# Kernel tuning notes

Hardware: AMD Instinct MI355X
Metric: run time of the kernel (lower is better)

## Reference

```python
import jax, jax.numpy as jnp
import numpy as np

B, T, IN, OUT, R = 4096, 8, 1024, 1024, 32

def setup_inputs() -> dict:
    key = jax.random.key(0)
    k1, k2, k3, k4 = jax.random.split(key, 4)
    return {
        "x": jax.random.normal(k1, (B, T, IN), dtype=jnp.float32),
        "first_shared_core": jax.random.normal(k2, (T, R), dtype=jnp.float32) * 0.1,
        "middle_shared_core": jax.random.normal(k3, (R, IN, R), dtype=jnp.float32) * 0.1,
        "task_core": jax.random.normal(k4, (R, OUT), dtype=jnp.float32) * 0.1,
    }

def reference(x, first_shared_core, middle_shared_core, task_core):
    # contract TT cores -> per-task weight [T, IN, OUT]
    w = jnp.einsum('tj,jik->tik', first_shared_core, middle_shared_core)
    w = jnp.einsum('tik,ko->tio', w, task_core)
    # per-task batched matmul: [B,T,IN] x [T,IN,OUT] -> [B,T,OUT]
    return jnp.einsum('bti,tio->bto', x, w)
```

## Files before the change

### kernel.cpp

```cpp
#include <hip/hip_runtime.h>
#include <hip/hip_bf16.h>
#include <stdint.h>

#define B_DIM 4096
#define T_DIM 8
#define IN_DIM 1024
#define OUT_DIM 1024
#define R_DIM 32

#define BM 128
#define BN 128
#define BK 64
#define NKT (IN_DIM / BK)

typedef __bf16 bf16x8 __attribute__((ext_vector_type(8)));
typedef float  f32x4  __attribute__((ext_vector_type(4)));


__device__ __forceinline__ uint32_t pack2_bf16(float a, float b) {
  uint32_t ua = __float_as_uint(a), ub = __float_as_uint(b);
  ua = (ua + 0x7FFFu + ((ua >> 16) & 1u)) >> 16;
  ub = (ub + 0x7FFFu + ((ub >> 16) & 1u)) & 0xFFFF0000u;
  return ua | ub;
}

__device__ __forceinline__ void gload_lds16(const void* g, void* l) {
  __builtin_amdgcn_global_load_lds(
      (const __attribute__((address_space(1))) void*)(uintptr_t)g,
      (__attribute__((address_space(3))) void*)(uint32_t)(uintptr_t)l,
      16, 0, 0);
}

__global__ void tt_stage1(const float* __restrict__ first,
                          const float* __restrict__ middle,
                          float* __restrict__ a1) {
  int idx = blockIdx.x * 256 + threadIdx.x;
  int t  = idx >> 15;
  int ik = idx & 32767;
  float acc = 0.f;
#pragma unroll
  for (int j = 0; j < R_DIM; ++j)
    acc = fmaf(first[t * R_DIM + j], middle[j * (IN_DIM * R_DIM) + ik], acc);
  a1[idx] = acc;
}

__global__ __launch_bounds__(256) void tt_stage2(const float* __restrict__ a1,
                                                 const float* __restrict__ task,
                                                 __hip_bfloat16* __restrict__ wT) {
  int bid = blockIdx.x;
  int t  = bid >> 8;
  int ob = (bid >> 4) & 15;
  int ib = bid & 15;
  __shared__ float A1s[64][33];
  __shared__ float Ts[32][64];
  int tid = threadIdx.x;
#pragma unroll
  for (int r = 0; r < 8; ++r) {
    int idx2 = tid + 256 * r;
    int il = idx2 >> 5, k = idx2 & 31;
    A1s[il][k] = a1[t * (IN_DIM * R_DIM) + (ib * 64 + il) * R_DIM + k];
  }
#pragma unroll
  for (int r = 0; r < 8; ++r) {
    int idx2 = tid + 256 * r;
    int k = idx2 >> 6, ol = idx2 & 63;
    Ts[k][ol] = task[k * OUT_DIM + ob * 64 + ol];
  }
  __syncthreads();
  int il = tid & 63;
  int og = tid >> 6;
  float acc[16];
#pragma unroll
  for (int r = 0; r < 16; ++r) acc[r] = 0.f;
#pragma unroll
  for (int k = 0; k < 32; ++k) {
    float a = A1s[il][k];
#pragma unroll
    for (int r = 0; r < 16; ++r)
      acc[r] = fmaf(a, Ts[k][og * 16 + r], acc[r]);
  }
#pragma unroll
  for (int r = 0; r < 16; ++r) {
    size_t o = (size_t)ob * 64 + og * 16 + r;
    wT[((size_t)t * OUT_DIM + o) * IN_DIM + ib * 64 + il] = __float2bfloat16(acc[r]);
  }
}

__global__ __launch_bounds__(256, 3) void tt_gemm(const float* __restrict__ X,
                                                  const uint16_t* __restrict__ WT,
                                                  float* __restrict__ O) {
  extern __shared__ uint8_t sm[];

  const int cpx = (T_DIM * (B_DIM / BM) * (OUT_DIM / BN)) >> 3;
  int bid = blockIdx.x;
  int l  = (bid & 7) * cpx + (bid >> 3);
  int t  = l >> 8;
  int mt = (l >> 3) & 31;
  int nt = l & 7;

  const int tid  = threadIdx.x;
  const int lane = tid & 63;
  const int wave = tid >> 6;
  const int wr = wave >> 1, wc = wave & 1;

  const int a_row  = tid >> 4;
  const int a_col4 = tid & 15;
  const float* xbase =
      X + ((size_t)(mt * BM) * T_DIM + t) * IN_DIM + a_col4 * 4;

  const int b_rowin = lane >> 3;
  const int b_c     = lane & 7;
  const int b_gcol  = (b_c * 16) ^ (b_rowin << 4);
  const uint16_t* wtile = WT + ((size_t)(t * OUT_DIM + nt * BN)) * IN_DIM;

  const int r0a  = wr * 64 + (lane & 15);
  const int r0b  = wc * 64 + (lane & 15);
  const int kswz = (lane & 7) << 4;
  const int kg   = lane >> 4;

  f32x4 acc[4][4] = {};
  float4 areg[8];

#pragma unroll
  for (int r = 0; r < 8; ++r)
    areg[r] = *(const float4*)(xbase + (size_t)(a_row + 16 * r) * (T_DIM * IN_DIM));

  for (int kt = 0; kt < NKT; ++kt) {
#pragma unroll
    for (int r = 0; r < 8; ++r) {
      int row = a_row + 16 * r;
      uint2 v;
      v.x = pack2_bf16(areg[r].x, areg[r].y);
      v.y = pack2_bf16(areg[r].z, areg[r].w);
      *(uint2*)(sm + row * 128 + ((a_col4 * 8) ^ ((row & 7) << 4))) = v;
    }
    {
      const uint16_t* wk = wtile + (size_t)kt * BK;
#pragma unroll
      for (int q = 0; q < 4; ++q) {
        int row = (wave * 4 + q) * 8 + b_rowin;
        gload_lds16((const uint8_t*)(wk + (size_t)row * IN_DIM) + b_gcol,
                    sm + 16384 + (wave * 4 + q) * 1024);
      }
    }
    __syncthreads();

    if (kt + 1 < NKT) {
      const float* xk = xbase + (size_t)(kt + 1) * BK;
#pragma unroll
      for (int r = 0; r < 8; ++r)
        areg[r] = *(const float4*)(xk + (size_t)(a_row + 16 * r) * (T_DIM * IN_DIM));
    }

    const uint8_t* ab = sm;
    const uint8_t* bb = sm + 16384;
#pragma unroll
    for (int ks = 0; ks < 2; ++ks) {
      const int kbyte = (ks * 64 + kg * 16) ^ kswz;
      bf16x8 af[4], bfr[4];
#pragma unroll
      for (int m = 0; m < 4; ++m)
        af[m] = *(const bf16x8*)(ab + (r0a + m * 16) * 128 + kbyte);
#pragma unroll
      for (int n = 0; n < 4; ++n)
        bfr[n] = *(const bf16x8*)(bb + (r0b + n * 16) * 128 + kbyte);
#pragma unroll
      for (int m = 0; m < 4; ++m)
#pragma unroll
        for (int n = 0; n < 4; ++n)
          acc[m][n] = __builtin_amdgcn_mfma_f32_16x16x32_bf16(af[m], bfr[n],
                                                              acc[m][n], 0, 0, 0);
    }
    __syncthreads();
  }

  const size_t obase =
      (size_t)(mt * BM) * (T_DIM * OUT_DIM) + (size_t)t * OUT_DIM + nt * BN;
  const int crow0 = wr * 64 + (lane >> 4) * 4;
  const int ccol  = wc * 64 + (lane & 15);
#pragma unroll
  for (int m = 0; m < 4; ++m) {
#pragma unroll
    for (int j = 0; j < 4; ++j) {
      size_t rowoff = obase + (size_t)(crow0 + m * 16 + j) * (T_DIM * OUT_DIM) + ccol;
#pragma unroll
      for (int n = 0; n < 4; ++n)
        O[rowoff + n * 16] = acc[m][n][j];
    }
  }
}

extern "C" void kernel_launch(void* const* d_in, const int* in_sizes, int n_in,
                              void* d_out, int out_size, void* d_ws, size_t ws_size,
                              hipStream_t stream) {
  const float* x      = (const float*)d_in[0];
  const float* first  = (const float*)d_in[1];
  const float* middle = (const float*)d_in[2];
  const float* task   = (const float*)d_in[3];
  float* out = (float*)d_out;

  float* a1 = (float*)d_ws;
  __hip_bfloat16* wT = (__hip_bfloat16*)((uint8_t*)d_ws + (1u << 20));

  tt_stage1<<<(T_DIM * IN_DIM * R_DIM) / 256, 256, 0, stream>>>(first, middle, a1);
  tt_stage2<<<T_DIM * 16 * 16, 256, 0, stream>>>(a1, task, wT);
  tt_gemm<<<T_DIM * (B_DIM / BM) * (OUT_DIM / BN), 256, 32768, stream>>>(
      x, (const uint16_t*)wT, out);
}
```

Baseline: 144.2 us.

## Stream fp32 X tiles directly to LDS and convert to bf16 at fragment load

The A operand (fp32 activations) is no longer loaded into registers, converted and written to LDS. It is now copied straight into a swizzled fp32 LDS tile with global_load_lds, and truncated to bf16 via byte-permute when each MFMA fragment is read. This removes the register staging and the round-to-nearest conversion from the load path. In exchange it doubles LDS use for A (48KB total), which may cut occupancy below the 3 blocks requested. It also drops the register prefetch of the next tile, and truncation replaces rounding, which slightly changes numerics.

```diff
diff --git a/kernel.cpp b/kernel.cpp
--- a/kernel.cpp
+++ b/kernel.cpp
@@ -16,13 +16,6 @@
 typedef __bf16 bf16x8 __attribute__((ext_vector_type(8)));
 typedef float  f32x4  __attribute__((ext_vector_type(4)));
 
-
-__device__ __forceinline__ uint32_t pack2_bf16(float a, float b) {
-  uint32_t ua = __float_as_uint(a), ub = __float_as_uint(b);
-  ua = (ua + 0x7FFFu + ((ua >> 16) & 1u)) >> 16;
-  ub = (ub + 0x7FFFu + ((ub >> 16) & 1u)) & 0xFFFF0000u;
-  return ua | ub;
-}
 
 __device__ __forceinline__ void gload_lds16(const void* g, void* l) {
   __builtin_amdgcn_global_load_lds(
@@ -103,67 +96,64 @@
   const int wave = tid >> 6;
   const int wr = wave >> 1, wc = wave & 1;
 
-  const int a_row  = tid >> 4;
-  const int a_col4 = tid & 15;
-  const float* xbase =
-      X + ((size_t)(mt * BM) * T_DIM + t) * IN_DIM + a_col4 * 4;
+  const int a_lrow   = lane >> 4;
+  const int a_lchunk = lane & 15;
+  const int srcf0 = (a_lchunk ^ a_lrow) * 4;
+  const int srcf1 = (a_lchunk ^ (4 + a_lrow)) * 4;
+  const float* xrow =
+      X + (size_t)(mt * BM + wave * 32 + a_lrow) * (T_DIM * IN_DIM) + t * IN_DIM;
 
   const int b_rowin = lane >> 3;
-  const int b_c     = lane & 7;
-  const int b_gcol  = (b_c * 16) ^ (b_rowin << 4);
+  const int b_gcol  = ((lane & 7) * 16) ^ (b_rowin << 4);
   const uint16_t* wtile = WT + ((size_t)(t * OUT_DIM + nt * BN)) * IN_DIM;
 
-  const int r0a  = wr * 64 + (lane & 15);
-  const int r0b  = wc * 64 + (lane & 15);
-  const int kswz = (lane & 7) << 4;
-  const int kg   = lane >> 4;
+  const int r0a = wr * 64 + (lane & 15);
+  const int r0b = wc * 64 + (lane & 15);
+  const int sA  = lane & 7;
+  const int kg  = lane >> 4;
+  const int kswzB = (lane & 7) << 4;
 
   f32x4 acc[4][4] = {};
-  float4 areg[8];
-
-#pragma unroll
-  for (int r = 0; r < 8; ++r)
-    areg[r] = *(const float4*)(xbase + (size_t)(a_row + 16 * r) * (T_DIM * IN_DIM));
 
   for (int kt = 0; kt < NKT; ++kt) {
+    const float* xk = xrow + kt * BK;
 #pragma unroll
-    for (int r = 0; r < 8; ++r) {
-      int row = a_row + 16 * r;
-      uint2 v;
-      v.x = pack2_bf16(areg[r].x, areg[r].y);
-      v.y = pack2_bf16(areg[r].z, areg[r].w);
-      *(uint2*)(sm + row * 128 + ((a_col4 * 8) ^ ((row & 7) << 4))) = v;
+    for (int qq = 0; qq < 8; ++qq) {
+      gload_lds16(xk + (size_t)qq * 4 * (T_DIM * IN_DIM) + ((qq & 1) ? srcf1 : srcf0),
+                  sm + (wave * 8 + qq) * 1024);
     }
-    {
-      const uint16_t* wk = wtile + (size_t)kt * BK;
+    const uint16_t* wk = wtile + (size_t)kt * BK;
 #pragma unroll
-      for (int q = 0; q < 4; ++q) {
-        int row = (wave * 4 + q) * 8 + b_rowin;
-        gload_lds16((const uint8_t*)(wk + (size_t)row * IN_DIM) + b_gcol,
-                    sm + 16384 + (wave * 4 + q) * 1024);
-      }
+    for (int q = 0; q < 4; ++q) {
+      int row = (wave * 4 + q) * 8 + b_rowin;
+      gload_lds16((const uint8_t*)(wk + (size_t)row * IN_DIM) + b_gcol,
+                  sm + 32768 + (wave * 4 + q) * 1024);
     }
     __syncthreads();
 
-    if (kt + 1 < NKT) {
-      const float* xk = xbase + (size_t)(kt + 1) * BK;
-#pragma unroll
-      for (int r = 0; r < 8; ++r)
-        areg[r] = *(const float4*)(xk + (size_t)(a_row + 16 * r) * (T_DIM * IN_DIM));
-    }
-
     const uint8_t* ab = sm;
-    const uint8_t* bb = sm + 16384;
+    const uint8_t* bb = sm + 32768;
 #pragma unroll
     for (int ks = 0; ks < 2; ++ks) {
-      const int kbyte = (ks * 64 + kg * 16) ^ kswz;
       bf16x8 af[4], bfr[4];
 #pragma unroll
-      for (int m = 0; m < 4; ++m)
-        af[m] = *(const bf16x8*)(ab + (r0a + m * 16) * 128 + kbyte);
+      for (int m = 0; m < 4; ++m) {
+        const int row = r0a + m * 16;
+        const int c0  = ks * 8 + kg * 2;
+        f32x4 lo = *(const f32x4*)(ab + row * 256 + (((c0    ) ^ sA) << 4));
+        f32x4 hi = *(const f32x4*)(ab + row * 256 + (((c0 + 1) ^ sA) << 4));
+        union { uint32_t u[4]; bf16x8 v; } cv;
+        cv.u[0] = __builtin_amdgcn_perm(__float_as_uint(lo.y), __float_as_uint(lo.x), 0x07060302u);
+        cv.u[1] = __builtin_amdgcn_perm(__float_as_uint(lo.w), __float_as_uint(lo.z), 0x07060302u);
+        cv.u[2] = __builtin_amdgcn_perm(__float_as_uint(hi.y), __float_as_uint(hi.x), 0x07060302u);
+        cv.u[3] = __builtin_amdgcn_perm(__float_as_uint(hi.w), __float_as_uint(hi.z), 0x07060302u);
+        af[m] = cv.v;
+      }
 #pragma unroll
-      for (int n = 0; n < 4; ++n)
+      for (int n = 0; n < 4; ++n) {
+        const int kbyte = (ks * 64 + kg * 16) ^ kswzB;
         bfr[n] = *(const bf16x8*)(bb + (r0b + n * 16) * 128 + kbyte);
+      }
 #pragma unroll
       for (int m = 0; m < 4; ++m)
 #pragma unroll
@@ -204,6 +194,6 @@
 
   tt_stage1<<<(T_DIM * IN_DIM * R_DIM) / 256, 256, 0, stream>>>(first, middle, a1);
   tt_stage2<<<T_DIM * 16 * 16, 256, 0, stream>>>(a1, task, wT);
-  tt_gemm<<<T_DIM * (B_DIM / BM) * (OUT_DIM / BN), 256, 32768, stream>>>(
+  tt_gemm<<<T_DIM * (B_DIM / BM) * (OUT_DIM / BN), 256, 49152, stream>>>(
       x, (const uint16_t*)wT, out);
 }
```

Result: faster. 139.5 us (-3.3%).

## Pre-convert X to bf16 and use 256x256 double-buffered 8-wave GEMM pipeline

Applied to the files above, without the earlier changes.

Adds a separate kernel that converts X to bf16 in a transposed [T,B,IN] layout, so the GEMM can load both operands straight into LDS with global_load_lds. The GEMM moves to 256x256 tiles with 8 waves and double-buffered 128KB LDS. Each k-step is split into four quadrant phases that interleave async loads for the next tile with MFMA bursts, using explicit vmcnt waits, barriers and setprio. The aim is to hide global-load latency and raise operand reuse per tile. In exchange it adds a full extra read and write pass over X and far fewer, larger workgroups (512 blocks).

```diff
diff --git a/kernel.cpp b/kernel.cpp
--- a/kernel.cpp
+++ b/kernel.cpp
@@ -8,13 +8,17 @@
 #define OUT_DIM 1024
 #define R_DIM 32
 
-#define BM 128
-#define BN 128
+#define BM 256
+#define BN 256
 #define BK 64
 #define NKT (IN_DIM / BK)
 
 typedef __bf16 bf16x8 __attribute__((ext_vector_type(8)));
 typedef float  f32x4  __attribute__((ext_vector_type(4)));
+
+#define VMCNT(n) asm volatile("s_waitcnt vmcnt(" #n ")" ::: "memory")
+#define CFENCE() asm volatile("" ::: "memory")
+#define BARRIER() do { CFENCE(); __builtin_amdgcn_s_barrier(); CFENCE(); } while (0)
 
 
 __device__ __forceinline__ uint32_t pack2_bf16(float a, float b) {
@@ -29,6 +33,43 @@
       (const __attribute__((address_space(1))) void*)(uintptr_t)g,
       (__attribute__((address_space(3))) void*)(uint32_t)(uintptr_t)l,
       16, 0, 0);
+}
+
+__device__ __forceinline__ void stage_half(const uint16_t* gtile, int ktn,
+                                           int half, uint8_t* ldsop,
+                                           int wave, int lane) {
+#pragma unroll
+  for (int j = 0; j < 2; ++j) {
+    int s = j * 64 + wave * 8 + (lane >> 3);
+    int c = lane & 7;
+    int row = (s >> 4) * 32 + half * 16 + (s & 15);
+    gload_lds16((const uint8_t*)(gtile + (size_t)row * IN_DIM + ktn * BK) +
+                    ((c ^ (s & 7)) << 4),
+                ldsop + half * 16384 + j * 8192 + wave * 1024);
+  }
+}
+
+__device__ __forceinline__ bf16x8 lds_frag(const uint8_t* op, int grp ,
+                                           int par , int ks,
+                                           int l15, int kg, int l7) {
+  return *(const bf16x8*)(op + par * 16384 + (grp >> 1) * 2048 + l15 * 128 +
+                          ((((ks << 2) + kg) ^ l7) << 4));
+}
+
+__global__ __launch_bounds__(256) void x_cvt(const float* __restrict__ x,
+                                             uint16_t* __restrict__ xb) {
+  int u = blockIdx.x * 256 + threadIdx.x;
+  int i0 = (u & 127) << 3;
+  int bt = u >> 7;
+  int t = bt & 7, b = bt >> 3;
+  const float4* src = (const float4*)(x + (size_t)bt * IN_DIM + i0);
+  float4 v0 = src[0], v1 = src[1];
+  uint4 o;
+  o.x = pack2_bf16(v0.x, v0.y);
+  o.y = pack2_bf16(v0.z, v0.w);
+  o.z = pack2_bf16(v1.x, v1.y);
+  o.w = pack2_bf16(v1.z, v1.w);
+  *(uint4*)(xb + ((size_t)t * B_DIM + b) * IN_DIM + i0) = o;
 }
 
 __global__ void tt_stage1(const float* __restrict__ first,
@@ -86,103 +127,132 @@
   }
 }
 
-__global__ __launch_bounds__(256, 3) void tt_gemm(const float* __restrict__ X,
+__global__ __launch_bounds__(512, 2) void tt_gemm(const uint16_t* __restrict__ XB,
                                                   const uint16_t* __restrict__ WT,
                                                   float* __restrict__ O) {
   extern __shared__ uint8_t sm[];
-
-  const int cpx = (T_DIM * (B_DIM / BM) * (OUT_DIM / BN)) >> 3;
   int bid = blockIdx.x;
-  int l  = (bid & 7) * cpx + (bid >> 3);
-  int t  = l >> 8;
-  int mt = (l >> 3) & 31;
-  int nt = l & 7;
+  const int t  = bid & 7;
+  const int l  = bid >> 3;
+  const int mt = l >> 2;
+  const int nt = l & 3;
 
   const int tid  = threadIdx.x;
   const int lane = tid & 63;
   const int wave = tid >> 6;
-  const int wr = wave >> 1, wc = wave & 1;
-
-  const int a_row  = tid >> 4;
-  const int a_col4 = tid & 15;
-  const float* xbase =
-      X + ((size_t)(mt * BM) * T_DIM + t) * IN_DIM + a_col4 * 4;
-
-  const int b_rowin = lane >> 3;
-  const int b_c     = lane & 7;
-  const int b_gcol  = (b_c * 16) ^ (b_rowin << 4);
-  const uint16_t* wtile = WT + ((size_t)(t * OUT_DIM + nt * BN)) * IN_DIM;
-
-  const int r0a  = wr * 64 + (lane & 15);
-  const int r0b  = wc * 64 + (lane & 15);
-  const int kswz = (lane & 7) << 4;
-  const int kg   = lane >> 4;
-
-  f32x4 acc[4][4] = {};
-  float4 areg[8];
-
-#pragma unroll
-  for (int r = 0; r < 8; ++r)
-    areg[r] = *(const float4*)(xbase + (size_t)(a_row + 16 * r) * (T_DIM * IN_DIM));
-
+  const int wr = wave >> 2, wc = wave & 3;
+  const int wr8 = wr * 8, wc4 = wc * 4;
+  const int l15 = lane & 15, l7 = lane & 7, kg = lane >> 4;
+
+  const uint16_t* gA = XB + ((size_t)t * B_DIM + mt * BM) * IN_DIM;
+  const uint16_t* gB = WT + ((size_t)t * OUT_DIM + nt * BN) * IN_DIM;
+
+  f32x4 acc[8][4] = {};
+  bf16x8 afr[4][2], bfr0[2][2], bfr1[2][2];
+
+  stage_half(gA, 0, 0, sm, wave, lane);
+  stage_half(gB, 0, 0, sm + 32768, wave, lane);
+  stage_half(gA, 0, 1, sm, wave, lane);
+  stage_half(gB, 0, 1, sm + 32768, wave, lane);
+  VMCNT(0);
+  BARRIER();
+
+#pragma unroll 2
   for (int kt = 0; kt < NKT; ++kt) {
-#pragma unroll
-    for (int r = 0; r < 8; ++r) {
-      int row = a_row + 16 * r;
-      uint2 v;
-      v.x = pack2_bf16(areg[r].x, areg[r].y);
-      v.y = pack2_bf16(areg[r].z, areg[r].w);
-      *(uint2*)(sm + row * 128 + ((a_col4 * 8) ^ ((row & 7) << 4))) = v;
-    }
-    {
-      const uint16_t* wk = wtile + (size_t)kt * BK;
-#pragma unroll
-      for (int q = 0; q < 4; ++q) {
-        int row = (wave * 4 + q) * 8 + b_rowin;
-        gload_lds16((const uint8_t*)(wk + (size_t)row * IN_DIM) + b_gcol,
-                    sm + 16384 + (wave * 4 + q) * 1024);
-      }
-    }
-    __syncthreads();
-
-    if (kt + 1 < NKT) {
-      const float* xk = xbase + (size_t)(kt + 1) * BK;
-#pragma unroll
-      for (int r = 0; r < 8; ++r)
-        areg[r] = *(const float4*)(xk + (size_t)(a_row + 16 * r) * (T_DIM * IN_DIM));
-    }
-
-    const uint8_t* ab = sm;
-    const uint8_t* bb = sm + 16384;
-#pragma unroll
-    for (int ks = 0; ks < 2; ++ks) {
-      const int kbyte = (ks * 64 + kg * 16) ^ kswz;
-      bf16x8 af[4], bfr[4];
-#pragma unroll
-      for (int m = 0; m < 4; ++m)
-        af[m] = *(const bf16x8*)(ab + (r0a + m * 16) * 128 + kbyte);
-#pragma unroll
-      for (int n = 0; n < 4; ++n)
-        bfr[n] = *(const bf16x8*)(bb + (r0b + n * 16) * 128 + kbyte);
-#pragma unroll
-      for (int m = 0; m < 4; ++m)
-#pragma unroll
-        for (int n = 0; n < 4; ++n)
-          acc[m][n] = __builtin_amdgcn_mfma_f32_16x16x32_bf16(af[m], bfr[n],
-                                                              acc[m][n], 0, 0, 0);
-    }
-    __syncthreads();
-  }
-
-  const size_t obase =
-      (size_t)(mt * BM) * (T_DIM * OUT_DIM) + (size_t)t * OUT_DIM + nt * BN;
-  const int crow0 = wr * 64 + (lane >> 4) * 4;
-  const int ccol  = wc * 64 + (lane & 15);
-#pragma unroll
-  for (int m = 0; m < 4; ++m) {
+    const int P = kt & 1;
+    const uint8_t* bA = sm + P * 65536;
+    const uint8_t* bB = bA + 32768;
+    uint8_t* nA = sm + (P ^ 1) * 65536;
+    uint8_t* nB = nA + 32768;
+    const bool st = (kt + 1) < NKT;
+
+#pragma unroll
+    for (int mo = 0; mo < 4; ++mo)
+#pragma unroll
+      for (int ks = 0; ks < 2; ++ks)
+        afr[mo][ks] = lds_frag(bA, wr8 + mo * 2, 0, ks, l15, kg, l7);
+#pragma unroll
+    for (int no = 0; no < 2; ++no)
+#pragma unroll
+      for (int ks = 0; ks < 2; ++ks)
+        bfr0[no][ks] = lds_frag(bB, wc4 + no * 2, 0, ks, l15, kg, l7);
+    if (st) stage_half(gA, kt + 1, 0, nA, wave, lane);
+    if (kt == NKT - 1) { VMCNT(0); } else { VMCNT(2); }
+    BARRIER();
+    __builtin_amdgcn_s_setprio(1);
+#pragma unroll
+    for (int mo = 0; mo < 4; ++mo)
+#pragma unroll
+      for (int no = 0; no < 2; ++no)
+#pragma unroll
+        for (int ks = 0; ks < 2; ++ks)
+          acc[mo * 2][no * 2] = __builtin_amdgcn_mfma_f32_16x16x32_bf16(
+              afr[mo][ks], bfr0[no][ks], acc[mo * 2][no * 2], 0, 0, 0);
+    __builtin_amdgcn_s_setprio(0);
+    BARRIER();
+
+#pragma unroll
+    for (int no = 0; no < 2; ++no)
+#pragma unroll
+      for (int ks = 0; ks < 2; ++ks)
+        bfr1[no][ks] = lds_frag(bB, wc4 + no * 2 + 1, 1, ks, l15, kg, l7);
+    if (st) stage_half(gB, kt + 1, 0, nB, wave, lane);
+    BARRIER();
+    __builtin_amdgcn_s_setprio(1);
+#pragma unroll
+    for (int mo = 0; mo < 4; ++mo)
+#pragma unroll
+      for (int no = 0; no < 2; ++no)
+#pragma unroll
+        for (int ks = 0; ks < 2; ++ks)
+          acc[mo * 2][no * 2 + 1] = __builtin_amdgcn_mfma_f32_16x16x32_bf16(
+              afr[mo][ks], bfr1[no][ks], acc[mo * 2][no * 2 + 1], 0, 0, 0);
+    __builtin_amdgcn_s_setprio(0);
+    BARRIER();
+
+#pragma unroll
+    for (int mo = 0; mo < 4; ++mo)
+#pragma unroll
+      for (int ks = 0; ks < 2; ++ks)
+        afr[mo][ks] = lds_frag(bA, wr8 + mo * 2 + 1, 1, ks, l15, kg, l7);
+    if (st) stage_half(gA, kt + 1, 1, nA, wave, lane);
+    BARRIER();
+    __builtin_amdgcn_s_setprio(1);
+#pragma unroll
+    for (int mo = 0; mo < 4; ++mo)
+#pragma unroll
+      for (int no = 0; no < 2; ++no)
+#pragma unroll
+        for (int ks = 0; ks < 2; ++ks)
+          acc[mo * 2 + 1][no * 2] = __builtin_amdgcn_mfma_f32_16x16x32_bf16(
+              afr[mo][ks], bfr0[no][ks], acc[mo * 2 + 1][no * 2], 0, 0, 0);
+    __builtin_amdgcn_s_setprio(0);
+    BARRIER();
+
+    if (st) stage_half(gB, kt + 1, 1, nB, wave, lane);
+    if (st) { VMCNT(4); }
+    BARRIER();
+    __builtin_amdgcn_s_setprio(1);
+#pragma unroll
+    for (int mo = 0; mo < 4; ++mo)
+#pragma unroll
+      for (int no = 0; no < 2; ++no)
+#pragma unroll
+        for (int ks = 0; ks < 2; ++ks)
+          acc[mo * 2 + 1][no * 2 + 1] = __builtin_amdgcn_mfma_f32_16x16x32_bf16(
+              afr[mo][ks], bfr1[no][ks], acc[mo * 2 + 1][no * 2 + 1], 0, 0, 0);
+    __builtin_amdgcn_s_setprio(0);
+    BARRIER();
+  }
+
+  const int crow0 = mt * BM + wr * 128 + (lane >> 4) * 4;
+  const int ccol0 = nt * BN + wc * 64 + (lane & 15);
+#pragma unroll
+  for (int m = 0; m < 8; ++m) {
 #pragma unroll
     for (int j = 0; j < 4; ++j) {
-      size_t rowoff = obase + (size_t)(crow0 + m * 16 + j) * (T_DIM * OUT_DIM) + ccol;
+      size_t rowoff =
+          ((size_t)(crow0 + m * 16 + j) * T_DIM + t) * OUT_DIM + ccol0;
 #pragma unroll
       for (int n = 0; n < 4; ++n)
         O[rowoff + n * 16] = acc[m][n][j];
@@ -201,9 +271,14 @@
 
   float* a1 = (float*)d_ws;
   __hip_bfloat16* wT = (__hip_bfloat16*)((uint8_t*)d_ws + (1u << 20));
-
+  uint16_t* xb = (uint16_t*)((uint8_t*)d_ws + (17u << 20));
+
+  hipFuncSetAttribute((const void*)tt_gemm,
+                      hipFuncAttributeMaxDynamicSharedMemorySize, 131072);
+
+  x_cvt<<<(B_DIM * T_DIM * IN_DIM) / 8 / 256, 256, 0, stream>>>(x, xb);
   tt_stage1<<<(T_DIM * IN_DIM * R_DIM) / 256, 256, 0, stream>>>(first, middle, a1);
   tt_stage2<<<T_DIM * 16 * 16, 256, 0, stream>>>(a1, task, wT);
-  tt_gemm<<<T_DIM * (B_DIM / BM) * (OUT_DIM / BN), 256, 32768, stream>>>(
-      x, (const uint16_t*)wT, out);
-}
+  tt_gemm<<<T_DIM * (B_DIM / BM) * (OUT_DIM / BN), 512, 131072, stream>>>(
+      xb, (const uint16_t*)wT, out);
+}
```

New measurement: 138.0 us. 4.3% less time.
